# Optimization experiments

Measured on AMD Instinct MI355X. Metric: run time of the kernel, lower is better.

Reference implementation:

```python
import jax, jax.numpy as jnp
import numpy as np

# Dims: B=2, S=2048, D=1024 hidden, E=8 experts, F=2752 ffn (SwiGLU), top-1 gate,
# capacity_factor=1.0 -> capacity C = (B*S)//E = 512. Residual-MoE (moe_use_residual=True).

def setup_inputs() -> dict:
    key = jax.random.key(0)
    ks = jax.random.split(key, 10)
    B, S, D, E, F = 2, 2048, 1024, 8, 2752
    sc = 0.02
    return {
        "hidden_states": jax.random.normal(ks[0], (B, S, D), jnp.float32),
        "wg":  jax.random.normal(ks[1], (D, E), jnp.float32) * sc,   # gate
        "w1":  jax.random.normal(ks[2], (E, D, F), jnp.float32) * sc,  # expert SwiGLU
        "w3":  jax.random.normal(ks[3], (E, D, F), jnp.float32) * sc,
        "w2":  jax.random.normal(ks[4], (E, F, D), jnp.float32) * sc,
        "rw1": jax.random.normal(ks[5], (D, F), jnp.float32) * sc,    # residual MLP (SwiGLU, no bias)
        "rw3": jax.random.normal(ks[6], (D, F), jnp.float32) * sc,
        "rw2": jax.random.normal(ks[7], (F, D), jnp.float32) * sc,
        "cw":  jax.random.normal(ks[8], (D, 2), jnp.float32) * sc,    # coefficient Linear(D, 2)
        "cb":  jnp.zeros((2,), jnp.float32),
    }


def _moe_forward(x, wg, w1, w3, w2):
    """GShard/DeepSpeed-style top-1 gated MoE with capacity + token dropping.
    x: [T, D] flattened tokens. Returns (out [T,D], l_aux scalar, exp_counts [E])."""
    T, D = x.shape
    E = wg.shape[1]
    C = max(4, T // E)  # capacity_factor = 1.0, min_capacity = 4

    logits = x @ wg                                  # [T, E]
    gates = jax.nn.softmax(logits, axis=-1)
    idx = jnp.argmax(gates, axis=-1)                 # top-1 expert per token
    mask1 = jax.nn.one_hot(idx, E, dtype=gates.dtype)  # [T, E]
    exp_counts = jnp.sum(mask1, axis=0).astype(jnp.int32)

    # load-balancing aux loss (DeepSpeed top1gating)
    me = jnp.mean(gates, axis=0)
    ce = jnp.mean(mask1, axis=0)
    l_aux = jnp.sum(me * ce) * E

    # position of each token within its expert's buffer; drop overflow
    locations = jnp.cumsum(mask1, axis=0) - 1.0      # [T, E]
    mask1 = mask1 * (locations < C)
    loc_s = jnp.sum(locations * mask1, axis=1).astype(jnp.int32)  # [T]
    gates1 = jnp.sum(gates * mask1, axis=1)          # [T] gate weight (0 if dropped)

    loc_oh = jax.nn.one_hot(loc_s, C, dtype=gates.dtype)          # [T, C]
    combine = gates1[:, None, None] * mask1[:, :, None] * loc_oh[:, None, :]  # [T, E, C]
    dispatch = (combine > 0).astype(x.dtype)

    xe = jnp.einsum("tec,td->ecd", dispatch, x)      # dispatch to [E, C, D]
    h = jax.nn.silu(jnp.einsum("ecd,edf->ecf", xe, w1)) * jnp.einsum("ecd,edf->ecf", xe, w3)
    ye = jnp.einsum("ecf,efd->ecd", h, w2)           # expert SwiGLU FFN
    out = jnp.einsum("tec,ecd->td", combine, ye)     # weighted combine back to tokens
    return out, l_aux, exp_counts


def reference(hidden_states, wg, w1, w3, w2, rw1, rw3, rw2, cw, cb):
    B, S, D = hidden_states.shape
    x = hidden_states.reshape(-1, D)
    moe_out, l_aux, exp_counts = _moe_forward(x, wg, w1, w3, w2)
    moe_out = moe_out.reshape(B, S, D)

    # residual SwiGLU MLP + softmax-gated combine (Residual-MoE)
    mlp = (jax.nn.silu(hidden_states @ rw1) * (hidden_states @ rw3)) @ rw2
    coef = jax.nn.softmax(hidden_states @ cw + cb, axis=-1)  # [B, S, 2]
    output = moe_out * coef[..., 0:1] + mlp * coef[..., 1:2]
    return output, l_aux, exp_counts
```

## Files before the change

kernel.cpp:

```cpp
#include <hip/hip_runtime.h>
#include <hip/hip_bf16.h>
#include <stdint.h>

#define T_TOK 4096
#define DD 1024
#define EE 8
#define CC 512
#define FF 2752
#define FP 2816

typedef __attribute__((ext_vector_type(8))) short bf16x8;
typedef __attribute__((ext_vector_type(4))) float f32x4;
typedef __attribute__((ext_vector_type(4))) unsigned short us4;

__device__ __forceinline__ float bf2f(unsigned short u) {
  union { float f; unsigned int i; } v; v.i = ((unsigned int)u) << 16; return v.f;
}
__device__ __forceinline__ unsigned short f2bf(float f) {
  union { float f; unsigned int i; } v; v.f = f;
  unsigned int r = v.i + 0x7fffu + ((v.i >> 16) & 1u);
  return (unsigned short)(r >> 16);
}

#define GLDS16(g, l) __builtin_amdgcn_global_load_lds( \
    (const __attribute__((address_space(1))) void*)(g), \
    (__attribute__((address_space(3))) void*)(l), 16, 0, 0)

#define STG_CHUNK(l) (((l & 3) ^ ((l >> 3) & 3)) * 8)
#define RD_OFF(fr, fq) ((fr) * 32 + (((fq) ^ (((fr) >> 1) & 3)) * 8))

#define BAR() do { asm volatile("" ::: "memory"); __builtin_amdgcn_s_barrier(); \
                   asm volatile("" ::: "memory"); } while (0)

__global__ __launch_bounds__(256)
void transpose_k(const float* __restrict__ in, const float* __restrict__ in2,
                 unsigned short* __restrict__ out, unsigned short* __restrict__ out2,
                 int R, int C, long inStride, long outStride) {
  __shared__ unsigned short sm[64][66];
  int b = blockIdx.z;
  if (b < EE) { in += (long)b * inStride; out += (long)b * outStride; }
  else { in = in2; out = out2; }
  int cb = blockIdx.x * 64, rb = blockIdx.y * 64;
  int t = threadIdx.x;
  int rr = t >> 4, c4 = (t & 15) * 4;
#pragma unroll
  for (int i = 0; i < 4; ++i) {
    int r = rr + i * 16;
    float4 v = *(const float4*)(in + (long)(rb + r) * C + cb + c4);
    us4 o; o.x = f2bf(v.x); o.y = f2bf(v.y); o.z = f2bf(v.z); o.w = f2bf(v.w);
    *(us4*)&sm[r][c4] = o;
  }
  __syncthreads();
  int r4 = (t & 15) * 4, cc = t >> 4;
#pragma unroll
  for (int i = 0; i < 4; ++i) {
    int c = cc + i * 16;
    us4 o;
    o.x = sm[r4 + 0][c]; o.y = sm[r4 + 1][c];
    o.z = sm[r4 + 2][c]; o.w = sm[r4 + 3][c];
    *(us4*)(out + (long)(cb + c) * R + rb + r4) = o;
  }
}

__global__ void zero_me_k(float* me) { if (threadIdx.x < EE) me[threadIdx.x] = 0.0f; }

__global__ void gate_k(const float* __restrict__ x, const float* __restrict__ wg,
                       const float* __restrict__ cw, const float* __restrict__ cbv,
                       int* __restrict__ idx, float* __restrict__ gatev,
                       float* __restrict__ coef, float* __restrict__ me_sum) {
  int tid = threadIdx.x, lane = tid & 63, wv = tid >> 6;
  int t = blockIdx.x * 4 + wv;
  const float* xr = x + (long)t * DD;
  float acc[EE] = {0,0,0,0,0,0,0,0};
  float c0 = 0.0f, c1 = 0.0f;
  for (int d = lane; d < DD; d += 64) {
    float xv = xr[d];
#pragma unroll
    for (int e = 0; e < EE; ++e) acc[e] += xv * wg[d * EE + e];
    c0 += xv * cw[d * 2 + 0];
    c1 += xv * cw[d * 2 + 1];
  }
#pragma unroll
  for (int o = 32; o > 0; o >>= 1) {
#pragma unroll
    for (int e = 0; e < EE; ++e) acc[e] += __shfl_xor(acc[e], o);
    c0 += __shfl_xor(c0, o);
    c1 += __shfl_xor(c1, o);
  }
  __shared__ float sme[EE];
  if (tid < EE) sme[tid] = 0.0f;
  __syncthreads();
  if (lane == 0) {
    float m = acc[0]; int am = 0;
#pragma unroll
    for (int e = 1; e < EE; ++e) if (acc[e] > m) { m = acc[e]; am = e; }
    float g[EE]; float s = 0.0f;
#pragma unroll
    for (int e = 0; e < EE; ++e) { g[e] = __expf(acc[e] - m); s += g[e]; }
    float inv = 1.0f / s;
    idx[t] = am;
    gatev[t] = g[am] * inv;
#pragma unroll
    for (int e = 0; e < EE; ++e) atomicAdd(&sme[e], g[e] * inv);
    float l0 = c0 + cbv[0], l1 = c1 + cbv[1];
    float mm = fmaxf(l0, l1);
    float e0 = __expf(l0 - mm), e1 = __expf(l1 - mm);
    float is = 1.0f / (e0 + e1);
    coef[t * 2 + 0] = e0 * is;
    coef[t * 2 + 1] = e1 * is;
  }
  __syncthreads();
  if (tid < EE) atomicAdd(&me_sum[tid], sme[tid]);
}

__global__ void scan_k(const int* __restrict__ idx, const float* __restrict__ me_sum,
                       int* __restrict__ slot, int* __restrict__ tok,
                       float* __restrict__ out_tail) {
  __shared__ int sidx[T_TOK];
  __shared__ int counts[EE];
  int tid = threadIdx.x;
  for (int i = tid; i < T_TOK; i += 512) sidx[i] = idx[i];
  __syncthreads();
  int e = tid >> 6, lane = tid & 63;
  int base = 0;
  for (int it = 0; it < T_TOK / 64; ++it) {
    int t = it * 64 + lane;
    bool f = (sidx[t] == e);
    unsigned long long m = __ballot(f);
    if (f) {
      int loc = base + __popcll(m & ((1ull << lane) - 1ull));
      slot[t] = (loc < CC) ? loc : -1;
      if (loc < CC) tok[e * CC + loc] = t;
    }
    base += __popcll(m);
  }
  if (lane == 0) counts[e] = base;
  __syncthreads();
  int filled = min(counts[e], CC);
  for (int c = filled + lane; c < CC; c += 64) tok[e * CC + c] = -1;
  if (tid == 0) {
    float la = 0.0f;
    for (int i = 0; i < EE; ++i) la += me_sum[i] * (float)counts[i];
    la *= (float)EE / ((float)T_TOK * (float)T_TOK);
    out_tail[0] = la;
    for (int i = 0; i < EE; ++i) out_tail[1 + i] = (float)counts[i];
  }
}

__global__ void gather_k(const float* __restrict__ x, const int* __restrict__ tok,
                         unsigned short* __restrict__ xb, unsigned short* __restrict__ xe) {
  int r = blockIdx.x, tid = threadIdx.x;
  int d = tid * 4;
  if (r < T_TOK) {
    float4 v = *(const float4*)(x + (long)r * DD + d);
    us4 o; o.x = f2bf(v.x); o.y = f2bf(v.y); o.z = f2bf(v.z); o.w = f2bf(v.w);
    *(us4*)(xb + (long)r * DD + d) = o;
  } else {
    int s = r - T_TOK;
    int t = tok[s];
    us4 o = {0, 0, 0, 0};
    if (t >= 0) {
      float4 v = *(const float4*)(x + (long)t * DD + d);
      o.x = f2bf(v.x); o.y = f2bf(v.y); o.z = f2bf(v.z); o.w = f2bf(v.w);
    }
    *(us4*)(xe + (long)s * DD + d) = o;
  }
}

__global__ __launch_bounds__(512, 2)
void gemm1_k(const unsigned short* __restrict__ xcat,
             const unsigned short* __restrict__ w1t, const unsigned short* __restrict__ w3t,
             const unsigned short* __restrict__ rw1t, const unsigned short* __restrict__ rw3t,
             unsigned short* __restrict__ Hcat) {
  int lin = blockIdx.x;
  int work = (lin & 7) * 88 + (lin >> 3);
  int mtile, ntile;
  if (work < 352) {
    int e = work / 44, r = work - e * 44;
    ntile = r >> 1;
    mtile = e * 2 + (r & 1);
  } else {
    int q = work - 352;
    ntile = q >> 4;
    mtile = 16 + (q & 15);
  }
  const unsigned short* A = xcat + (size_t)mtile * 256 * DD;
  const unsigned short *B1, *B3;
  if (mtile < 16) { int e = mtile >> 1; B1 = w1t + (size_t)e * FP * DD; B3 = w3t + (size_t)e * FP * DD; }
  else { B1 = rw1t; B3 = rw3t; }
  unsigned short* H = Hcat + (size_t)mtile * 256 * FF;
  int n0 = ntile * 128;

  __shared__ __align__(16) unsigned short lds[65536];
  char* L = (char*)lds;

  int tid = threadIdx.x, l = tid & 63, w = tid >> 6;
  int wm = w >> 1, wn = w & 1;
  int fr = l & 15, fq = l >> 4;
  int srow = l >> 2, soff = STG_CHUNK(l);
  int rdo = RD_OFF(fr, fq);

  const unsigned short* gA0 = A + (size_t)(w * 16 + srow) * DD + soff;
  const unsigned short* gA1 = A + (size_t)((8 + w) * 16 + srow) * DD + soff;
  const unsigned short* gB1 = B1 + (size_t)(n0 + w * 16 + srow) * DD + soff;
  const unsigned short* gB3 = B3 + (size_t)(n0 + w * 16 + srow) * DD + soff;

#define STAGE1(slot, kt, ks) do { int kk = (kt) * 64 + (ks) * 32;                      \
    GLDS16(gA0 + kk, L + (slot) * 32768 + (ks) * 16384 + w * 1024);                    \
    GLDS16(gA1 + kk, L + (slot) * 32768 + (ks) * 16384 + (8 + w) * 1024);              \
    GLDS16(gB1 + kk, L + 65536 + (slot) * 16384 + (ks) * 8192 + w * 1024);             \
    GLDS16(gB3 + kk, L + 98304 + (slot) * 16384 + (ks) * 8192 + w * 1024); } while (0)

  f32x4 acc1[4][4] = {};
  f32x4 acc3[4][4] = {};

  const int NT = DD / 64;
  STAGE1(0, 0, 0);
  STAGE1(0, 0, 1);
  STAGE1(1, 1, 0);

  for (int t = 0; t < NT; ++t) {
    int slot = t & 1, nslot = slot ^ 1;
    int t1 = (t + 1 < NT) ? t + 1 : 0;
    int t2 = (t + 2 < NT) ? t + 2 : t + 2 - NT;
    bf16x8 af[4], bf[4];

    asm volatile("s_waitcnt vmcnt(8)" ::: "memory");
    BAR();
#pragma unroll
    for (int mi = 0; mi < 4; ++mi)
      af[mi] = *(const bf16x8*)(lds + slot * 16384 + (wm * 4 + mi) * 512 + rdo);
#pragma unroll
    for (int ni = 0; ni < 4; ++ni)
      bf[ni] = *(const bf16x8*)(lds + 32768 + slot * 8192 + (wn * 4 + ni) * 512 + rdo);
    STAGE1(nslot, t1, 1);
    __builtin_amdgcn_s_setprio(1);
#pragma unroll
    for (int mi = 0; mi < 4; ++mi)
#pragma unroll
      for (int ni = 0; ni < 4; ++ni)
        acc1[mi][ni] = __builtin_amdgcn_mfma_f32_16x16x32_bf16(af[mi], bf[ni], acc1[mi][ni], 0, 0, 0);
    __builtin_amdgcn_s_setprio(0);

#pragma unroll
    for (int ni = 0; ni < 4; ++ni)
      bf[ni] = *(const bf16x8*)(lds + 49152 + slot * 8192 + (wn * 4 + ni) * 512 + rdo);
    __builtin_amdgcn_s_setprio(1);
#pragma unroll
    for (int mi = 0; mi < 4; ++mi)
#pragma unroll
      for (int ni = 0; ni < 4; ++ni)
        acc3[mi][ni] = __builtin_amdgcn_mfma_f32_16x16x32_bf16(af[mi], bf[ni], acc3[mi][ni], 0, 0, 0);
    __builtin_amdgcn_s_setprio(0);

    asm volatile("s_waitcnt vmcnt(8)" ::: "memory");
    BAR();
#pragma unroll
    for (int mi = 0; mi < 4; ++mi)
      af[mi] = *(const bf16x8*)(lds + slot * 16384 + 8192 + (wm * 4 + mi) * 512 + rdo);
#pragma unroll
    for (int ni = 0; ni < 4; ++ni)
      bf[ni] = *(const bf16x8*)(lds + 32768 + slot * 8192 + 4096 + (wn * 4 + ni) * 512 + rdo);
    STAGE1(slot, t2, 0);
    __builtin_amdgcn_s_setprio(1);
#pragma unroll
    for (int mi = 0; mi < 4; ++mi)
#pragma unroll
      for (int ni = 0; ni < 4; ++ni)
        acc1[mi][ni] = __builtin_amdgcn_mfma_f32_16x16x32_bf16(af[mi], bf[ni], acc1[mi][ni], 0, 0, 0);
    __builtin_amdgcn_s_setprio(0);

#pragma unroll
    for (int ni = 0; ni < 4; ++ni)
      bf[ni] = *(const bf16x8*)(lds + 49152 + slot * 8192 + 4096 + (wn * 4 + ni) * 512 + rdo);
    __builtin_amdgcn_s_setprio(1);
#pragma unroll
    for (int mi = 0; mi < 4; ++mi)
#pragma unroll
      for (int ni = 0; ni < 4; ++ni)
        acc3[mi][ni] = __builtin_amdgcn_mfma_f32_16x16x32_bf16(af[mi], bf[ni], acc3[mi][ni], 0, 0, 0);
    __builtin_amdgcn_s_setprio(0);
  }
#undef STAGE1

#pragma unroll
  for (int mi = 0; mi < 4; ++mi)
#pragma unroll
    for (int ni = 0; ni < 4; ++ni)
#pragma unroll
      for (int r = 0; r < 4; ++r) {
        int gm = wm * 64 + mi * 16 + fq * 4 + r;
        int gn = n0 + wn * 64 + ni * 16 + fr;
        if (gn < FF) {
          float v1 = acc1[mi][ni][r], v3 = acc3[mi][ni][r];
          float h = v1 / (1.0f + __expf(-v1)) * v3;
          H[(size_t)gm * FF + gn] = f2bf(h);
        }
      }
}

__global__ __launch_bounds__(512, 2)
void gemm2_k(const unsigned short* __restrict__ Hcat,
             const unsigned short* __restrict__ w2t, const unsigned short* __restrict__ rw2t,
             unsigned short* __restrict__ Ycat) {
  int lin = blockIdx.x;
  int work = (lin & 7) * 32 + (lin >> 3);
  int mtile, ntile;
  if (work < 128) {
    int e = work >> 4, r = work & 15;
    ntile = r >> 1;
    mtile = e * 2 + (r & 1);
  } else {
    int q = work - 128;
    ntile = q >> 4;
    mtile = 16 + (q & 15);
  }
  const unsigned short* A = Hcat + (size_t)mtile * 256 * FF;
  const unsigned short* B = (mtile < 16) ? (w2t + (size_t)(mtile >> 1) * DD * FF) : rw2t;
  unsigned short* Y = Ycat + (size_t)mtile * 256 * DD;
  int n0 = ntile * 128;

  __shared__ __align__(16) unsigned short lds[49152];
  char* L = (char*)lds;

  int tid = threadIdx.x, l = tid & 63, w = tid >> 6;
  int wm = w >> 1, wn = w & 1;
  int fr = l & 15, fq = l >> 4;
  int srow = l >> 2, soff = STG_CHUNK(l);
  int rdo = RD_OFF(fr, fq);

  const unsigned short* gA0 = A + (size_t)(w * 16 + srow) * FF + soff;
  const unsigned short* gA1 = A + (size_t)((8 + w) * 16 + srow) * FF + soff;
  const unsigned short* gB  = B + (size_t)(n0 + w * 16 + srow) * FF + soff;

#define STAGE2(slot, kt, ks) do { int kk = (kt) * 64 + (ks) * 32;                      \
    GLDS16(gA0 + kk, L + (slot) * 32768 + (ks) * 16384 + w * 1024);                    \
    GLDS16(gA1 + kk, L + (slot) * 32768 + (ks) * 16384 + (8 + w) * 1024);              \
    GLDS16(gB  + kk, L + 65536 + (slot) * 16384 + (ks) * 8192 + w * 1024); } while (0)

  f32x4 acc[4][4] = {};

  const int NT = FF / 64;
  STAGE2(0, 0, 0);
  STAGE2(0, 0, 1);
  STAGE2(1, 1, 0);

  for (int t = 0; t < NT; ++t) {
    int slot = t & 1, nslot = slot ^ 1;
    int t1 = (t + 1 < NT) ? t + 1 : 0;
    int t2 = (t + 2 < NT) ? t + 2 : t + 2 - NT;
    bf16x8 af[4], bf[4];

    asm volatile("s_waitcnt vmcnt(6)" ::: "memory");
    BAR();
#pragma unroll
    for (int mi = 0; mi < 4; ++mi)
      af[mi] = *(const bf16x8*)(lds + slot * 16384 + (wm * 4 + mi) * 512 + rdo);
#pragma unroll
    for (int ni = 0; ni < 4; ++ni)
      bf[ni] = *(const bf16x8*)(lds + 32768 + slot * 8192 + (wn * 4 + ni) * 512 + rdo);
    STAGE2(nslot, t1, 1);
    __builtin_amdgcn_s_setprio(1);
#pragma unroll
    for (int mi = 0; mi < 4; ++mi)
#pragma unroll
      for (int ni = 0; ni < 4; ++ni)
        acc[mi][ni] = __builtin_amdgcn_mfma_f32_16x16x32_bf16(af[mi], bf[ni], acc[mi][ni], 0, 0, 0);
    __builtin_amdgcn_s_setprio(0);

    asm volatile("s_waitcnt vmcnt(6)" ::: "memory");
    BAR();
#pragma unroll
    for (int mi = 0; mi < 4; ++mi)
      af[mi] = *(const bf16x8*)(lds + slot * 16384 + 8192 + (wm * 4 + mi) * 512 + rdo);
#pragma unroll
    for (int ni = 0; ni < 4; ++ni)
      bf[ni] = *(const bf16x8*)(lds + 32768 + slot * 8192 + 4096 + (wn * 4 + ni) * 512 + rdo);
    STAGE2(slot, t2, 0);
    __builtin_amdgcn_s_setprio(1);
#pragma unroll
    for (int mi = 0; mi < 4; ++mi)
#pragma unroll
      for (int ni = 0; ni < 4; ++ni)
        acc[mi][ni] = __builtin_amdgcn_mfma_f32_16x16x32_bf16(af[mi], bf[ni], acc[mi][ni], 0, 0, 0);
    __builtin_amdgcn_s_setprio(0);
  }
#undef STAGE2

#pragma unroll
  for (int mi = 0; mi < 4; ++mi)
#pragma unroll
    for (int ni = 0; ni < 4; ++ni)
#pragma unroll
      for (int r = 0; r < 4; ++r) {
        int gm = wm * 64 + mi * 16 + fq * 4 + r;
        int gn = n0 + wn * 64 + ni * 16 + fr;
        Y[(size_t)gm * DD + gn] = f2bf(acc[mi][ni][r]);
      }
}

__global__ void combine_k(const unsigned short* __restrict__ Ye, const unsigned short* __restrict__ Yr,
                          const int* __restrict__ idx, const int* __restrict__ slot,
                          const float* __restrict__ gatev, const float* __restrict__ coef,
                          float* __restrict__ out) {
  int t = blockIdx.x, tid = threadIdx.x;
  int d = tid * 4;
  float c0 = coef[t * 2], c1 = coef[t * 2 + 1];
  int s = slot[t];
  float g = gatev[t] * c0;
  us4 vr = *(const us4*)(Yr + (size_t)t * DD + d);
  float4 o;
  if (s >= 0) {
    us4 ve = *(const us4*)(Ye + ((size_t)idx[t] * CC + s) * DD + d);
    o.x = g * bf2f(ve.x) + c1 * bf2f(vr.x);
    o.y = g * bf2f(ve.y) + c1 * bf2f(vr.y);
    o.z = g * bf2f(ve.z) + c1 * bf2f(vr.z);
    o.w = g * bf2f(ve.w) + c1 * bf2f(vr.w);
  } else {
    o.x = c1 * bf2f(vr.x);
    o.y = c1 * bf2f(vr.y);
    o.z = c1 * bf2f(vr.z);
    o.w = c1 * bf2f(vr.w);
  }
  *(float4*)(out + (size_t)t * DD + d) = o;
}

extern "C" void kernel_launch(void* const* d_in, const int* in_sizes, int n_in,
                              void* d_out, int out_size, void* d_ws, size_t ws_size,
                              hipStream_t stream) {
  const float* x   = (const float*)d_in[0];
  const float* wg  = (const float*)d_in[1];
  const float* w1  = (const float*)d_in[2];
  const float* w3  = (const float*)d_in[3];
  const float* w2  = (const float*)d_in[4];
  const float* rw1 = (const float*)d_in[5];
  const float* rw3 = (const float*)d_in[6];
  const float* rw2 = (const float*)d_in[7];
  const float* cw  = (const float*)d_in[8];
  const float* cbv = (const float*)d_in[9];
  float* out = (float*)d_out;

  char* ws = (char*)d_ws;
  size_t o = 0;
  auto alloc = [&](size_t bytes) -> char* {
    char* p = ws + o; o = (o + bytes + 255) & ~(size_t)255; return p;
  };
  unsigned short* w1t  = (unsigned short*)alloc((size_t)EE * FP * DD * 2);
  unsigned short* w3t  = (unsigned short*)alloc((size_t)EE * FP * DD * 2);
  unsigned short* w2t  = (unsigned short*)alloc((size_t)EE * DD * FF * 2);
  unsigned short* rw1t = (unsigned short*)alloc((size_t)FP * DD * 2);
  unsigned short* rw3t = (unsigned short*)alloc((size_t)FP * DD * 2);
  unsigned short* rw2t = (unsigned short*)alloc((size_t)DD * FF * 2);
  unsigned short* xe   = (unsigned short*)alloc((size_t)T_TOK * DD * 2);
  unsigned short* xb   = (unsigned short*)alloc((size_t)T_TOK * DD * 2);
  unsigned short* He   = (unsigned short*)alloc((size_t)T_TOK * FF * 2);
  unsigned short* Hr   = (unsigned short*)alloc((size_t)T_TOK * FF * 2);
  unsigned short* Ye   = (unsigned short*)alloc((size_t)T_TOK * DD * 2);
  unsigned short* Yr   = (unsigned short*)alloc((size_t)T_TOK * DD * 2);
  int*   idxp  = (int*)alloc(T_TOK * 4);
  float* gatev = (float*)alloc(T_TOK * 4);
  int*   slotp = (int*)alloc(T_TOK * 4);
  int*   tokp  = (int*)alloc(EE * CC * 4);
  float* coefp = (float*)alloc(T_TOK * 2 * 4);
  float* mep   = (float*)alloc(256);
  if (o > ws_size) return;

  transpose_k<<<dim3(43, 16, EE + 1), 256, 0, stream>>>(w1, rw1, w1t, rw1t, DD, FF, (long)DD * FF, (long)FP * DD);
  transpose_k<<<dim3(43, 16, EE + 1), 256, 0, stream>>>(w3, rw3, w3t, rw3t, DD, FF, (long)DD * FF, (long)FP * DD);
  transpose_k<<<dim3(16, 43, EE + 1), 256, 0, stream>>>(w2, rw2, w2t, rw2t, FF, DD, (long)FF * DD, (long)DD * FF);

  zero_me_k<<<1, 64, 0, stream>>>(mep);
  gate_k<<<T_TOK / 4, 256, 0, stream>>>(x, wg, cw, cbv, idxp, gatev, coefp, mep);
  scan_k<<<1, 512, 0, stream>>>(idxp, mep, slotp, tokp, out + (size_t)T_TOK * DD);
  gather_k<<<2 * T_TOK, 256, 0, stream>>>(x, tokp, xb, xe);
  gemm1_k<<<704, 512, 0, stream>>>(xe, w1t, w3t, rw1t, rw3t, He);
  gemm2_k<<<256, 512, 0, stream>>>(He, w2t, rw2t, Ye);
  combine_k<<<T_TOK, 256, 0, stream>>>(Ye, Yr, idxp, slotp, gatev, coefp, out);
}
```

Measured before the change: 302.2 us.

## Restructure GEMM pipelines and widen transpose tiles with XOR-swizzled LDS

Three changes land together. The weight transpose kernel becomes a template on row-tile height, with 128-row tiles for w1/w3, an XOR-swizzled shared buffer instead of padding, and 16-byte output stores. gemm1 now splits staging of A and B across sub-steps with one-stage-ahead prefetch and extra barriers around each MFMA block. gemm2 moves to a 3-slot LDS ring with two-ahead prefetch and a larger shared buffer. The aim is to hide global-load latency and speed up weight conversion, at the cost of more barriers in gemm1 and more LDS use in gemm2, which may reduce occupancy.

```diff
diff --git a/kernel.cpp b/kernel.cpp
--- a/kernel.cpp
+++ b/kernel.cpp
@@ -12,6 +12,7 @@
 typedef __attribute__((ext_vector_type(8))) short bf16x8;
 typedef __attribute__((ext_vector_type(4))) float f32x4;
 typedef __attribute__((ext_vector_type(4))) unsigned short us4;
+typedef __attribute__((ext_vector_type(8))) unsigned short us8;
 
 __device__ __forceinline__ float bf2f(unsigned short u) {
   union { float f; unsigned int i; } v; v.i = ((unsigned int)u) << 16; return v.f;
@@ -32,33 +33,40 @@
 #define BAR() do { asm volatile("" ::: "memory"); __builtin_amdgcn_s_barrier(); \
                    asm volatile("" ::: "memory"); } while (0)
 
+template<int RT>
 __global__ __launch_bounds__(256)
 void transpose_k(const float* __restrict__ in, const float* __restrict__ in2,
                  unsigned short* __restrict__ out, unsigned short* __restrict__ out2,
                  int R, int C, long inStride, long outStride) {
-  __shared__ unsigned short sm[64][66];
+  __shared__ unsigned short sm[RT * 64];
   int b = blockIdx.z;
   if (b < EE) { in += (long)b * inStride; out += (long)b * outStride; }
   else { in = in2; out = out2; }
-  int cb = blockIdx.x * 64, rb = blockIdx.y * 64;
+  int cb = blockIdx.x * 64, rb = blockIdx.y * RT;
   int t = threadIdx.x;
   int rr = t >> 4, c4 = (t & 15) * 4;
 #pragma unroll
-  for (int i = 0; i < 4; ++i) {
+  for (int i = 0; i < RT / 16; ++i) {
     int r = rr + i * 16;
     float4 v = *(const float4*)(in + (long)(rb + r) * C + cb + c4);
     us4 o; o.x = f2bf(v.x); o.y = f2bf(v.y); o.z = f2bf(v.z); o.w = f2bf(v.w);
-    *(us4*)&sm[r][c4] = o;
+    *(us4*)&sm[r * 64 + (c4 ^ (((r >> 3) & 7) << 3))] = o;
   }
   __syncthreads();
-  int r4 = (t & 15) * 4, cc = t >> 4;
-#pragma unroll
-  for (int i = 0; i < 4; ++i) {
-    int c = cc + i * 16;
-    us4 o;
-    o.x = sm[r4 + 0][c]; o.y = sm[r4 + 1][c];
-    o.z = sm[r4 + 2][c]; o.w = sm[r4 + 3][c];
-    *(us4*)(out + (long)(cb + c) * R + rb + r4) = o;
+#pragma unroll
+  for (int j = 0; j < (64 * (RT / 8)) / 256; ++j) {
+    int idx = t + j * 256;
+    int g, c;
+    if (RT == 128) { g = idx & 15; c = idx >> 4; }
+    else           { g = idx & 7;  c = idx >> 3; }
+    int r8 = g * 8;
+    us8 o;
+#pragma unroll
+    for (int k = 0; k < 8; ++k) {
+      int r = r8 + k;
+      o[k] = sm[r * 64 + (c ^ (((r >> 3) & 7) << 3))];
+    }
+    *(us8*)(out + (long)(cb + c) * R + rb + r8) = o;
   }
 }
 
@@ -205,83 +213,90 @@
   const unsigned short* gB1 = B1 + (size_t)(n0 + w * 16 + srow) * DD + soff;
   const unsigned short* gB3 = B3 + (size_t)(n0 + w * 16 + srow) * DD + soff;
 
-#define STAGE1(slot, kt, ks) do { int kk = (kt) * 64 + (ks) * 32;                      \
-    GLDS16(gA0 + kk, L + (slot) * 32768 + (ks) * 16384 + w * 1024);                    \
-    GLDS16(gA1 + kk, L + (slot) * 32768 + (ks) * 16384 + (8 + w) * 1024);              \
-    GLDS16(gB1 + kk, L + 65536 + (slot) * 16384 + (ks) * 8192 + w * 1024);             \
-    GLDS16(gB3 + kk, L + 98304 + (slot) * 16384 + (ks) * 8192 + w * 1024); } while (0)
+#define STG_A(ss, kk, ks) do {                                                    \
+    GLDS16(gA0 + (kk) + (ks) * 32, L + (ss) * 32768 + (ks) * 16384 + w * 1024);   \
+    GLDS16(gA1 + (kk) + (ks) * 32, L + (ss) * 32768 + (ks) * 16384 + (8 + w) * 1024); } while (0)
+#define STG_B(ss, kk, ks) do {                                                    \
+    GLDS16(gB1 + (kk) + (ks) * 32, L + 65536 + (ss) * 16384 + (ks) * 8192 + w * 1024); \
+    GLDS16(gB3 + (kk) + (ks) * 32, L + 98304 + (ss) * 16384 + (ks) * 8192 + w * 1024); } while (0)
 
   f32x4 acc1[4][4] = {};
   f32x4 acc3[4][4] = {};
+  bf16x8 af[4], b1f[4], b3f[4];
 
   const int NT = DD / 64;
-  STAGE1(0, 0, 0);
-  STAGE1(0, 0, 1);
-  STAGE1(1, 1, 0);
+  STG_A(0, 0, 0); STG_B(0, 0, 0); STG_A(0, 0, 1); STG_B(0, 0, 1);
 
   for (int t = 0; t < NT; ++t) {
-    int slot = t & 1, nslot = slot ^ 1;
-    int t1 = (t + 1 < NT) ? t + 1 : 0;
-    int t2 = (t + 2 < NT) ? t + 2 : t + 2 - NT;
-    bf16x8 af[4], bf[4];
-
-    asm volatile("s_waitcnt vmcnt(8)" ::: "memory");
-    BAR();
-#pragma unroll
-    for (int mi = 0; mi < 4; ++mi)
-      af[mi] = *(const bf16x8*)(lds + slot * 16384 + (wm * 4 + mi) * 512 + rdo);
-#pragma unroll
-    for (int ni = 0; ni < 4; ++ni)
-      bf[ni] = *(const bf16x8*)(lds + 32768 + slot * 8192 + (wn * 4 + ni) * 512 + rdo);
-    STAGE1(nslot, t1, 1);
-    __builtin_amdgcn_s_setprio(1);
-#pragma unroll
-    for (int mi = 0; mi < 4; ++mi)
-#pragma unroll
-      for (int ni = 0; ni < 4; ++ni)
-        acc1[mi][ni] = __builtin_amdgcn_mfma_f32_16x16x32_bf16(af[mi], bf[ni], acc1[mi][ni], 0, 0, 0);
-    __builtin_amdgcn_s_setprio(0);
-
-#pragma unroll
-    for (int ni = 0; ni < 4; ++ni)
-      bf[ni] = *(const bf16x8*)(lds + 49152 + slot * 8192 + (wn * 4 + ni) * 512 + rdo);
-    __builtin_amdgcn_s_setprio(1);
-#pragma unroll
-    for (int mi = 0; mi < 4; ++mi)
-#pragma unroll
-      for (int ni = 0; ni < 4; ++ni)
-        acc3[mi][ni] = __builtin_amdgcn_mfma_f32_16x16x32_bf16(af[mi], bf[ni], acc3[mi][ni], 0, 0, 0);
-    __builtin_amdgcn_s_setprio(0);
-
-    asm volatile("s_waitcnt vmcnt(8)" ::: "memory");
-    BAR();
-#pragma unroll
-    for (int mi = 0; mi < 4; ++mi)
-      af[mi] = *(const bf16x8*)(lds + slot * 16384 + 8192 + (wm * 4 + mi) * 512 + rdo);
-#pragma unroll
-    for (int ni = 0; ni < 4; ++ni)
-      bf[ni] = *(const bf16x8*)(lds + 32768 + slot * 8192 + 4096 + (wn * 4 + ni) * 512 + rdo);
-    STAGE1(slot, t2, 0);
-    __builtin_amdgcn_s_setprio(1);
-#pragma unroll
-    for (int mi = 0; mi < 4; ++mi)
-#pragma unroll
-      for (int ni = 0; ni < 4; ++ni)
-        acc1[mi][ni] = __builtin_amdgcn_mfma_f32_16x16x32_bf16(af[mi], bf[ni], acc1[mi][ni], 0, 0, 0);
-    __builtin_amdgcn_s_setprio(0);
-
-#pragma unroll
-    for (int ni = 0; ni < 4; ++ni)
-      bf[ni] = *(const bf16x8*)(lds + 49152 + slot * 8192 + 4096 + (wn * 4 + ni) * 512 + rdo);
-    __builtin_amdgcn_s_setprio(1);
-#pragma unroll
-    for (int mi = 0; mi < 4; ++mi)
-#pragma unroll
-      for (int ni = 0; ni < 4; ++ni)
-        acc3[mi][ni] = __builtin_amdgcn_mfma_f32_16x16x32_bf16(af[mi], bf[ni], acc3[mi][ni], 0, 0, 0);
-    __builtin_amdgcn_s_setprio(0);
-  }
-#undef STAGE1
+    int s = t & 1, ns = s ^ 1;
+    int kk1 = ((t + 1 < NT) ? t + 1 : 0) * 64;
+
+    STG_A(ns, kk1, 0);
+    asm volatile("s_waitcnt vmcnt(6)" ::: "memory");
+#pragma unroll
+    for (int mi = 0; mi < 4; ++mi)
+      af[mi] = *(const bf16x8*)(lds + s * 16384 + (wm * 4 + mi) * 512 + rdo);
+#pragma unroll
+    for (int ni = 0; ni < 4; ++ni)
+      b1f[ni] = *(const bf16x8*)(lds + 32768 + s * 8192 + (wn * 4 + ni) * 512 + rdo);
+    BAR();
+    __builtin_amdgcn_s_setprio(1);
+#pragma unroll
+    for (int mi = 0; mi < 4; ++mi)
+#pragma unroll
+      for (int ni = 0; ni < 4; ++ni)
+        acc1[mi][ni] = __builtin_amdgcn_mfma_f32_16x16x32_bf16(af[mi], b1f[ni], acc1[mi][ni], 0, 0, 0);
+    __builtin_amdgcn_s_setprio(0);
+    BAR();
+
+#pragma unroll
+    for (int ni = 0; ni < 4; ++ni)
+      b3f[ni] = *(const bf16x8*)(lds + 49152 + s * 8192 + (wn * 4 + ni) * 512 + rdo);
+    STG_B(ns, kk1, 0);
+    BAR();
+    __builtin_amdgcn_s_setprio(1);
+#pragma unroll
+    for (int mi = 0; mi < 4; ++mi)
+#pragma unroll
+      for (int ni = 0; ni < 4; ++ni)
+        acc3[mi][ni] = __builtin_amdgcn_mfma_f32_16x16x32_bf16(af[mi], b3f[ni], acc3[mi][ni], 0, 0, 0);
+    __builtin_amdgcn_s_setprio(0);
+    BAR();
+
+    STG_A(ns, kk1, 1);
+    asm volatile("s_waitcnt vmcnt(6)" ::: "memory");
+#pragma unroll
+    for (int mi = 0; mi < 4; ++mi)
+      af[mi] = *(const bf16x8*)(lds + s * 16384 + 8192 + (wm * 4 + mi) * 512 + rdo);
+#pragma unroll
+    for (int ni = 0; ni < 4; ++ni)
+      b1f[ni] = *(const bf16x8*)(lds + 32768 + s * 8192 + 4096 + (wn * 4 + ni) * 512 + rdo);
+    BAR();
+    __builtin_amdgcn_s_setprio(1);
+#pragma unroll
+    for (int mi = 0; mi < 4; ++mi)
+#pragma unroll
+      for (int ni = 0; ni < 4; ++ni)
+        acc1[mi][ni] = __builtin_amdgcn_mfma_f32_16x16x32_bf16(af[mi], b1f[ni], acc1[mi][ni], 0, 0, 0);
+    __builtin_amdgcn_s_setprio(0);
+    BAR();
+
+#pragma unroll
+    for (int ni = 0; ni < 4; ++ni)
+      b3f[ni] = *(const bf16x8*)(lds + 49152 + s * 8192 + 4096 + (wn * 4 + ni) * 512 + rdo);
+    STG_B(ns, kk1, 1);
+    BAR();
+    __builtin_amdgcn_s_setprio(1);
+#pragma unroll
+    for (int mi = 0; mi < 4; ++mi)
+#pragma unroll
+      for (int ni = 0; ni < 4; ++ni)
+        acc3[mi][ni] = __builtin_amdgcn_mfma_f32_16x16x32_bf16(af[mi], b3f[ni], acc3[mi][ni], 0, 0, 0);
+    __builtin_amdgcn_s_setprio(0);
+    BAR();
+  }
+#undef STG_A
+#undef STG_B
 
 #pragma unroll
   for (int mi = 0; mi < 4; ++mi)
@@ -320,7 +335,7 @@
   unsigned short* Y = Ycat + (size_t)mtile * 256 * DD;
   int n0 = ntile * 128;
 
-  __shared__ __align__(16) unsigned short lds[49152];
+  __shared__ __align__(16) unsigned short lds[73728];
   char* L = (char*)lds;
 
   int tid = threadIdx.x, l = tid & 63, w = tid >> 6;
@@ -333,33 +348,33 @@
   const unsigned short* gA1 = A + (size_t)((8 + w) * 16 + srow) * FF + soff;
   const unsigned short* gB  = B + (size_t)(n0 + w * 16 + srow) * FF + soff;
 
-#define STAGE2(slot, kt, ks) do { int kk = (kt) * 64 + (ks) * 32;                      \
-    GLDS16(gA0 + kk, L + (slot) * 32768 + (ks) * 16384 + w * 1024);                    \
-    GLDS16(gA1 + kk, L + (slot) * 32768 + (ks) * 16384 + (8 + w) * 1024);              \
-    GLDS16(gB  + kk, L + 65536 + (slot) * 16384 + (ks) * 8192 + w * 1024); } while (0)
+#define STG2(ss, kk, ks) do {                                                        \
+    GLDS16(gA0 + (kk) + (ks) * 32, L + (ss) * 32768 + (ks) * 16384 + w * 1024);      \
+    GLDS16(gA1 + (kk) + (ks) * 32, L + (ss) * 32768 + (ks) * 16384 + (8 + w) * 1024);\
+    GLDS16(gB  + (kk) + (ks) * 32, L + 98304 + (ss) * 16384 + (ks) * 8192 + w * 1024); } while (0)
 
   f32x4 acc[4][4] = {};
+  bf16x8 af[4], bf[4];
 
   const int NT = FF / 64;
-  STAGE2(0, 0, 0);
-  STAGE2(0, 0, 1);
-  STAGE2(1, 1, 0);
+  STG2(0, 0, 0); STG2(0, 0, 1);
+  STG2(1, 64, 0); STG2(1, 64, 1);
 
   for (int t = 0; t < NT; ++t) {
-    int slot = t & 1, nslot = slot ^ 1;
-    int t1 = (t + 1 < NT) ? t + 1 : 0;
-    int t2 = (t + 2 < NT) ? t + 2 : t + 2 - NT;
-    bf16x8 af[4], bf[4];
-
-    asm volatile("s_waitcnt vmcnt(6)" ::: "memory");
-    BAR();
-#pragma unroll
-    for (int mi = 0; mi < 4; ++mi)
-      af[mi] = *(const bf16x8*)(lds + slot * 16384 + (wm * 4 + mi) * 512 + rdo);
-#pragma unroll
-    for (int ni = 0; ni < 4; ++ni)
-      bf[ni] = *(const bf16x8*)(lds + 32768 + slot * 8192 + (wn * 4 + ni) * 512 + rdo);
-    STAGE2(nslot, t1, 1);
+    int st = t % 3;
+    int t2 = t + 2; if (t2 >= NT) t2 -= NT;
+    int st2 = (st + 2) % 3;
+    int kk2 = t2 * 64;
+
+    STG2(st2, kk2, 0);
+    asm volatile("s_waitcnt vmcnt(12)" ::: "memory");
+#pragma unroll
+    for (int mi = 0; mi < 4; ++mi)
+      af[mi] = *(const bf16x8*)(lds + st * 16384 + (wm * 4 + mi) * 512 + rdo);
+#pragma unroll
+    for (int ni = 0; ni < 4; ++ni)
+      bf[ni] = *(const bf16x8*)(lds + 49152 + st * 8192 + (wn * 4 + ni) * 512 + rdo);
+    BAR();
     __builtin_amdgcn_s_setprio(1);
 #pragma unroll
     for (int mi = 0; mi < 4; ++mi)
@@ -367,16 +382,17 @@
       for (int ni = 0; ni < 4; ++ni)
         acc[mi][ni] = __builtin_amdgcn_mfma_f32_16x16x32_bf16(af[mi], bf[ni], acc[mi][ni], 0, 0, 0);
     __builtin_amdgcn_s_setprio(0);
-
-    asm volatile("s_waitcnt vmcnt(6)" ::: "memory");
-    BAR();
-#pragma unroll
-    for (int mi = 0; mi < 4; ++mi)
-      af[mi] = *(const bf16x8*)(lds + slot * 16384 + 8192 + (wm * 4 + mi) * 512 + rdo);
-#pragma unroll
-    for (int ni = 0; ni < 4; ++ni)
-      bf[ni] = *(const bf16x8*)(lds + 32768 + slot * 8192 + 4096 + (wn * 4 + ni) * 512 + rdo);
-    STAGE2(slot, t2, 0);
+    BAR();
+
+    STG2(st2, kk2, 1);
+    asm volatile("s_waitcnt vmcnt(12)" ::: "memory");
+#pragma unroll
+    for (int mi = 0; mi < 4; ++mi)
+      af[mi] = *(const bf16x8*)(lds + st * 16384 + 8192 + (wm * 4 + mi) * 512 + rdo);
+#pragma unroll
+    for (int ni = 0; ni < 4; ++ni)
+      bf[ni] = *(const bf16x8*)(lds + 49152 + st * 8192 + 4096 + (wn * 4 + ni) * 512 + rdo);
+    BAR();
     __builtin_amdgcn_s_setprio(1);
 #pragma unroll
     for (int mi = 0; mi < 4; ++mi)
@@ -384,8 +400,9 @@
       for (int ni = 0; ni < 4; ++ni)
         acc[mi][ni] = __builtin_amdgcn_mfma_f32_16x16x32_bf16(af[mi], bf[ni], acc[mi][ni], 0, 0, 0);
     __builtin_amdgcn_s_setprio(0);
-  }
-#undef STAGE2
+    BAR();
+  }
+#undef STG2
 
 #pragma unroll
   for (int mi = 0; mi < 4; ++mi)
@@ -465,9 +482,9 @@
   float* mep   = (float*)alloc(256);
   if (o > ws_size) return;
 
-  transpose_k<<<dim3(43, 16, EE + 1), 256, 0, stream>>>(w1, rw1, w1t, rw1t, DD, FF, (long)DD * FF, (long)FP * DD);
-  transpose_k<<<dim3(43, 16, EE + 1), 256, 0, stream>>>(w3, rw3, w3t, rw3t, DD, FF, (long)DD * FF, (long)FP * DD);
-  transpose_k<<<dim3(16, 43, EE + 1), 256, 0, stream>>>(w2, rw2, w2t, rw2t, FF, DD, (long)FF * DD, (long)DD * FF);
+  transpose_k<128><<<dim3(43, 8, EE + 1), 256, 0, stream>>>(w1, rw1, w1t, rw1t, DD, FF, (long)DD * FF, (long)FP * DD);
+  transpose_k<128><<<dim3(43, 8, EE + 1), 256, 0, stream>>>(w3, rw3, w3t, rw3t, DD, FF, (long)DD * FF, (long)FP * DD);
+  transpose_k<64><<<dim3(16, 43, EE + 1), 256, 0, stream>>>(w2, rw2, w2t, rw2t, FF, DD, (long)FF * DD, (long)DD * FF);
 
   zero_me_k<<<1, 64, 0, stream>>>(mep);
   gate_k<<<T_TOK / 4, 256, 0, stream>>>(x, wg, cw, cbv, idxp, gatev, coefp, mep);
```

New measurement: 302.0 us. About the same (-0.0%).
